# Performance work log

Hardware: AMD Instinct MI355X
Metric: run time of the kernel (lower is better)

The kernel has to match this reference:

```python
import jax, jax.numpy as jnp
import numpy as np

K_NN = 9  # kernel_size: neighbors per node (includes self, dist 0)


def knn_edges(feat):
    """feat: (B, C, N). Replicates DenseDilatedKnnGraph (dilation=1):
    L2-normalize over channels, dense pairwise sq-distance, top-k nearest."""
    nrm = jnp.sqrt(jnp.sum(feat * feat, axis=1, keepdims=True))
    xn = feat / jnp.maximum(nrm, 1e-12)            # F.normalize(dim=1)
    xt = jnp.swapaxes(xn, 1, 2)                    # (B, N, C)
    sq = jnp.sum(xt * xt, axis=-1)                 # (B, N)
    dist = sq[:, :, None] + sq[:, None, :] - 2.0 * jnp.einsum('bnc,bmc->bnm', xt, xt)
    _, nn_idx = jax.lax.top_k(-dist, K_NN)         # (B, N, k)
    center = jnp.broadcast_to(jnp.arange(nn_idx.shape[1], dtype=nn_idx.dtype)[None, :, None], nn_idx.shape)
    return nn_idx, center                          # (x_j sources, x_i targets)


def reference(x, W0, W1, bias):
    B, C, H, W = x.shape
    N = H * W
    NB = B * N
    feat = x.reshape(B, C, N)
    # KNN graph is built on detached features in the torch source
    x_j, x_i = knn_edges(jax.lax.stop_gradient(feat))
    E = B * N * K_NN
    # faithful to source: torch.linspace(0, B, steps=E, dtype=int64) batch offsets
    count = jnp.linspace(0.0, float(B), E).astype(jnp.int32)
    src = x_j.reshape(-1).astype(jnp.int32) + count * N
    dst = x_i.reshape(-1).astype(jnp.int32) + count * N
    valid = (src < NB) & (dst < NB)                # drop the out-of-range tail edge
    # flat_nodes: (B, C, H, W) -> (B*H*W, C), node id = b*HW + pixel
    nodes = jnp.swapaxes(feat, 1, 2).reshape(NB, C)
    # ChebConv K=2, sym norm, lambda_max=2: Tx0 = x, Tx1 = -(D^-1/2 A D^-1/2) x
    w = valid.astype(nodes.dtype)
    deg = jax.ops.segment_sum(w, src, num_segments=NB)
    dinv = jnp.where(deg > 0, jax.lax.rsqrt(jnp.maximum(deg, 1.0)), 0.0)
    norm = -(dinv[src] * w * dinv[dst])            # scaled-Laplacian edge weights
    msg = norm[:, None] * nodes[src]               # (E, C) gather + weight
    Tx1 = jax.ops.segment_sum(msg, dst, num_segments=NB)
    return nodes @ W0 + Tx1 @ W1 + bias


def setup_inputs() -> dict:
    key = jax.random.key(0)
    k1, k2, k3, k4 = jax.random.split(key, 4)
    B, C, H, W = 8, 48, 64, 64
    Cout = 48
    s = 1.0 / np.sqrt(C)
    return {
        'x': jax.random.normal(k1, (B, C, H, W), dtype=jnp.float32),
        'W0': jax.random.normal(k2, (C, Cout), dtype=jnp.float32) * s,
        'W1': jax.random.normal(k3, (C, Cout), dtype=jnp.float32) * s,
        'bias': jax.random.normal(k4, (Cout,), dtype=jnp.float32) * 0.01,
    }
```

## Files before the change

### kernel.cpp

```cpp
#include <hip/hip_runtime.h>

#define BATCH 8
#define CH    48
#define NPTS  4096
#define NBN   (BATCH*NPTS)
#define KNN   9
#define NCAND 12

typedef unsigned short u16;
typedef unsigned int   u32;
typedef unsigned long long u64;
typedef __bf16 bf16x8 __attribute__((ext_vector_type(8)));
typedef float  f32x4  __attribute__((ext_vector_type(4)));

__device__ __forceinline__ float bf2f(u16 v) { return __uint_as_float(((u32)v) << 16); }
__device__ __forceinline__ u16 f2bf(float f) {
  u32 u = __float_as_uint(f);
  u = (u + 0x7fffu + ((u >> 16) & 1u)) >> 16;
  return (u16)u;
}

#define MED3U(d, a, b, c) \
  asm("v_med3_u32 %0, %1, %2, %3" : "=v"(d) : "v"(a), "v"(b), "v"(c))
#define INS12(p0,p1,p2,p3,p4,p5,p6,p7,p8,p9,p10,p11,x) do { \
  MED3U(p11,p10,p11,x); MED3U(p10,p9,p10,x); MED3U(p9,p8,p9,x);  \
  MED3U(p8, p7, p8, x); MED3U(p7, p6,p7, x); MED3U(p6,p5,p6,x);  \
  MED3U(p5, p4, p5, x); MED3U(p4, p3,p4, x); MED3U(p3,p2,p3,x);  \
  MED3U(p2, p1, p2, x); MED3U(p1, p0,p1, x); p0 = min(p0, x);    \
} while (0)

__device__ __forceinline__ void stage_q(const u16* g, u16* l) {
  __builtin_amdgcn_global_load_lds(
      (const __attribute__((address_space(1))) void*)g,
      (__attribute__((address_space(3))) void*)l, 16, 0, 0);
}

__global__ __launch_bounds__(64)
void k_prep(const float* __restrict__ x, float* __restrict__ xraw,
            float* __restrict__ xn, float* __restrict__ csq,
            u16* __restrict__ Abuf, u16* __restrict__ Bbuf,
            int* __restrict__ deg) {
  int node = blockIdx.x * 64 + threadIdx.x;
  deg[node] = 0;
  int b = node >> 12, n = node & (NPTS - 1);
  const float* xb = x + (size_t)b * CH * NPTS;
  float f[CH];
#pragma unroll
  for (int c = 0; c < CH; ++c) f[c] = xb[(size_t)c * NPTS + n];
  float a0 = 0, a1 = 0, a2 = 0, a3 = 0;
#pragma unroll
  for (int k = 0; k < CH; k += 4) {
    a0 += f[k] * f[k]; a1 += f[k+1] * f[k+1];
    a2 += f[k+2] * f[k+2]; a3 += f[k+3] * f[k+3];
  }
  float nrm = fmaxf(sqrtf((a0 + a1) + (a2 + a3)), 1e-12f);
  float rn = 1.0f / nrm;
  a0 = a1 = a2 = a3 = 0;
#pragma unroll
  for (int k = 0; k < CH; k += 4) {
    float v0 = f[k]*rn, v1 = f[k+1]*rn, v2 = f[k+2]*rn, v3 = f[k+3]*rn;
    a0 += v0*v0; a1 += v1*v1; a2 += v2*v2; a3 += v3*v3;
  }
  float csqv = (a0 + a1) + (a2 + a3);
  csq[node] = csqv;
  float4* ro = (float4*)(xraw + (size_t)node * CH);
  float4* no = (float4*)(xn   + (size_t)node * CH);
#pragma unroll
  for (int i = 0; i < CH / 4; ++i) {
    ro[i] = make_float4(f[4*i], f[4*i+1], f[4*i+2], f[4*i+3]);
    no[i] = make_float4(f[4*i]*rn, f[4*i+1]*rn, f[4*i+2]*rn, f[4*i+3]*rn);
  }
  uint4* Bo = (uint4*)(Bbuf + (size_t)node * 128);
  u16* Ag = Abuf + (size_t)(node >> 4) * 2048 + (size_t)(node & 15) * 8;
#pragma unroll
  for (int g = 0; g < 6; ++g) {
    u32 bhw[4], blw[4], ahw[4], alw[4];
#pragma unroll
    for (int j = 0; j < 4; ++j) {
      int k = g * 8 + j * 2;
      float v0 = f[k] * rn, v1 = f[k+1] * rn;
      u16 h0 = f2bf(v0), h1 = f2bf(v1);
      u16 l0 = f2bf(v0 - bf2f(h0)), l1 = f2bf(v1 - bf2f(h1));
      bhw[j] = (u32)h0 | ((u32)h1 << 16);
      blw[j] = (u32)l0 | ((u32)l1 << 16);
      float w0 = -2.0f * v0, w1 = -2.0f * v1;
      u16 g0 = f2bf(w0), g1 = f2bf(w1);
      u16 m0 = f2bf(w0 - bf2f(g0)), m1 = f2bf(w1 - bf2f(g1));
      ahw[j] = (u32)g0 | ((u32)g1 << 16);
      alw[j] = (u32)m0 | ((u32)m1 << 16);
    }
    Bo[g]     = make_uint4(bhw[0], bhw[1], bhw[2], bhw[3]);
    Bo[8 + g] = make_uint4(blw[0], blw[1], blw[2], blw[3]);
    int v = g >> 2, q = g & 3;
    *(uint4*)(Ag + v * 512 + q * 128)        = make_uint4(ahw[0], ahw[1], ahw[2], ahw[3]);
    *(uint4*)(Ag + 1024 + v * 512 + q * 128) = make_uint4(alw[0], alw[1], alw[2], alw[3]);
  }
  {
    u16 h = f2bf(csqv); u16 l = f2bf(csqv - bf2f(h));
    Bo[6]  = make_uint4(0x3F80u, 0, 0, 0);
    Bo[14] = make_uint4(0, 0, 0, 0);
    *(uint4*)(Ag + 512 + 2 * 128)        = make_uint4((u32)h, 0, 0, 0);
    *(uint4*)(Ag + 1024 + 512 + 2 * 128) = make_uint4((u32)l, 0, 0, 0);
  }
  {
    uint4 z = make_uint4(0, 0, 0, 0);
    Bo[7] = z; Bo[15] = z;
    *(uint4*)(Ag + 512 + 3 * 128)        = z;
    *(uint4*)(Ag + 1024 + 512 + 3 * 128) = z;
  }
}

__global__ __launch_bounds__(256, 6)
void k_knn_m(const u16* __restrict__ Abuf, const u16* __restrict__ Bbuf,
             u32* __restrict__ candu) {
  __shared__ __align__(16) u16 As[2][2][2048];
  int tid = threadIdx.x;
  int lane = tid & 63;
  int wv = tid >> 6;
  int quad = lane >> 4, m16 = lane & 15;
  int panel = blockIdx.x * 4 + wv;
  int row = panel * 16 + m16;
  int b4096 = row & ~(NPTS - 1);
  int half = blockIdx.y;
  int ct0 = half * 128;

  const __bf16* Bb = (const __bf16*)Bbuf + (size_t)row * 128;
  bf16x8 bh0 = *(const bf16x8*)(Bb + quad * 8);
  bf16x8 bh1 = *(const bf16x8*)(Bb + 32 + quad * 8);
  bf16x8 bl0 = *(const bf16x8*)(Bb + 64 + quad * 8);
  bf16x8 bl1 = *(const bf16x8*)(Bb + 96 + quad * 8);

  const u16* gs = Abuf + ((size_t)(b4096 >> 4) + ct0) * 2048
                  + wv * 512 + lane * 8;

  u32 s0=~0u,s1=~0u,s2=~0u,s3=~0u,s4=~0u,s5=~0u,
      s6=~0u,s7=~0u,s8=~0u,s9=~0u,s10=~0u,s11=~0u;

  const f32x4 C25 = {2.5f, 2.5f, 2.5f, 2.5f};

#define LDA(P, S, A0,A1,A2,A3) do {                                         \
    const u16* _p = &As[P][S][lane * 8];                                    \
    A0 = *(const bf16x8*)(_p);                                              \
    A1 = *(const bf16x8*)(_p + 512);                                        \
    A2 = *(const bf16x8*)(_p + 1024);                                       \
    A3 = *(const bf16x8*)(_p + 1536);                                       \
  } while (0)
#define MFMA6(ACC, A0,A1,A2,A3) do {                                        \
    ACC = __builtin_amdgcn_mfma_f32_16x16x32_bf16(A0, bh0, C25, 0, 0, 0);   \
    ACC = __builtin_amdgcn_mfma_f32_16x16x32_bf16(A1, bh1, ACC, 0, 0, 0);   \
    ACC = __builtin_amdgcn_mfma_f32_16x16x32_bf16(A0, bl0, ACC, 0, 0, 0);   \
    ACC = __builtin_amdgcn_mfma_f32_16x16x32_bf16(A1, bl1, ACC, 0, 0, 0);   \
    ACC = __builtin_amdgcn_mfma_f32_16x16x32_bf16(A2, bh0, ACC, 0, 0, 0);   \
    ACC = __builtin_amdgcn_mfma_f32_16x16x32_bf16(A3, bh1, ACC, 0, 0, 0);   \
  } while (0)
#define FILTER(ACC, CT) do {                                                \
    u32 _colb = ((u32)(CT) << 4) | ((u32)quad << 2);                        \
    _Pragma("unroll")                                                       \
    for (int _r = 0; _r < 4; ++_r) {                                        \
      u32 _u = __float_as_uint((ACC)[_r]);                                  \
      u32 _x = (_u & 0xFFFFF000u) | (_colb | (u32)_r);                      \
      INS12(s0,s1,s2,s3,s4,s5,s6,s7,s8,s9,s10,s11, _x);                     \
    }                                                                       \
  } while (0)

  f32x4 accA, accB;
  bf16x8 a0, a1, a2, a3;

  stage_q(gs,        &As[0][0][wv * 512]);
  stage_q(gs + 2048, &As[0][1][wv * 512]);
  __syncthreads();

  LDA(0, 0, a0, a1, a2, a3);
  stage_q(gs + (size_t)2 * 2048, &As[1][0][wv * 512]);
  stage_q(gs + (size_t)3 * 2048, &As[1][1][wv * 512]);
  MFMA6(accA, a0, a1, a2, a3);
  LDA(0, 1, a0, a1, a2, a3);
  MFMA6(accB, a0, a1, a2, a3);
  FILTER(accA, ct0 + 0);
  __syncthreads();

  for (int p = 1; p < 63; ++p) {
    int par = p & 1;
    LDA(par, 0, a0, a1, a2, a3);
    stage_q(gs + (size_t)(2 * p + 2) * 2048, &As[par ^ 1][0][wv * 512]);
    stage_q(gs + (size_t)(2 * p + 3) * 2048, &As[par ^ 1][1][wv * 512]);
    MFMA6(accA, a0, a1, a2, a3);
    FILTER(accB, ct0 + 2 * p - 1);
    LDA(par, 1, a0, a1, a2, a3);
    MFMA6(accB, a0, a1, a2, a3);
    FILTER(accA, ct0 + 2 * p);
    __syncthreads();
  }
  LDA(1, 0, a0, a1, a2, a3);
  MFMA6(accA, a0, a1, a2, a3);
  FILTER(accB, ct0 + 125);
  LDA(1, 1, a0, a1, a2, a3);
  MFMA6(accB, a0, a1, a2, a3);
  FILTER(accA, ct0 + 126);
  FILTER(accB, ct0 + 127);
#undef LDA
#undef MFMA6
#undef FILTER

  u32* o = candu + (((size_t)row * 2 + half) * 4 + quad) * NCAND;
  o[0]=s0; o[1]=s1; o[2]=s2; o[3]=s3; o[4]=s4; o[5]=s5;
  o[6]=s6; o[7]=s7; o[8]=s8; o[9]=s9; o[10]=s10; o[11]=s11;
}

#define RWS 32
__global__ __launch_bounds__(256)
void k_rr(const u32* __restrict__ candu, const float* __restrict__ xn,
          const float* __restrict__ csq, u16* __restrict__ nn,
          int* __restrict__ deg) {
  __shared__ __align__(16) u32 cs[RWS][48];
  __shared__ __align__(16) float xnS[RWS][52];
  __shared__ float csqS[RWS];
  __shared__ float dS[RWS][12];
  __shared__ int   iS[RWS][12];
  int tid = threadIdx.x, bi = blockIdx.x;
  int row0 = (bi & 7) * NPTS + (bi >> 3) * RWS;
  int b4096 = row0 & ~(NPTS - 1);
  for (int i = tid; i < RWS * 12; i += 256) {
    int ln = i / 12, f4 = i % 12;
    *(float4*)&xnS[ln][f4 * 4] =
        *(const float4*)(xn + (size_t)(row0 + ln) * CH + f4 * 4);
  }
  if (tid < RWS) csqS[tid] = csq[row0 + tid];
  if (tid < RWS * 4) {
    int lr = tid >> 2, q = tid & 3;
    const uint4* src = (const uint4*)(candu + (size_t)(row0 + lr) * 96 + q * 24);
    u32 t0=~0u,t1=~0u,t2=~0u,t3=~0u,t4=~0u,t5=~0u,
        t6=~0u,t7=~0u,t8=~0u,t9=~0u,t10=~0u,t11=~0u;
#pragma unroll
    for (int s = 0; s < 6; ++s) {
      uint4 v = src[s];
      INS12(t0,t1,t2,t3,t4,t5,t6,t7,t8,t9,t10,t11, v.x);
      INS12(t0,t1,t2,t3,t4,t5,t6,t7,t8,t9,t10,t11, v.y);
      INS12(t0,t1,t2,t3,t4,t5,t6,t7,t8,t9,t10,t11, v.z);
      INS12(t0,t1,t2,t3,t4,t5,t6,t7,t8,t9,t10,t11, v.w);
    }
    u32* lw = &cs[lr][q * 12];
    lw[0]=t0; lw[1]=t1; lw[2]=t2; lw[3]=t3; lw[4]=t4; lw[5]=t5;
    lw[6]=t6; lw[7]=t7; lw[8]=t8; lw[9]=t9; lw[10]=t10; lw[11]=t11;
  }
  __syncthreads();
  if (tid < RWS) {
    int lr = tid;
    u32 g0=~0u,g1=~0u,g2=~0u,g3=~0u,g4=~0u,g5=~0u,
        g6=~0u,g7=~0u,g8=~0u,g9=~0u,g10=~0u,g11=~0u;
    const uint4* ls4 = (const uint4*)&cs[lr][0];
#pragma unroll
    for (int s = 0; s < 12; ++s) {
      uint4 v = ls4[s];
      INS12(g0,g1,g2,g3,g4,g5,g6,g7,g8,g9,g10,g11, v.x);
      INS12(g0,g1,g2,g3,g4,g5,g6,g7,g8,g9,g10,g11, v.y);
      INS12(g0,g1,g2,g3,g4,g5,g6,g7,g8,g9,g10,g11, v.z);
      INS12(g0,g1,g2,g3,g4,g5,g6,g7,g8,g9,g10,g11, v.w);
    }
    u32* lw = &cs[lr][0];
    lw[0]=g0; lw[1]=g1; lw[2]=g2; lw[3]=g3; lw[4]=g4; lw[5]=g5;
    lw[6]=g6; lw[7]=g7; lw[8]=g8; lw[9]=g9; lw[10]=g10; lw[11]=g11;
  }
  __syncthreads();
  for (int task = tid; task < RWS * 12; task += 256) {
    int r = task / 12, j = task % 12;
    int c = (int)(cs[r][j] & 0xFFFu);
    const float4* cp = (const float4*)(xn + (size_t)(b4096 + c) * CH);
    const float* rf = &xnS[r][0];
    float a0 = 0, a1 = 0, a2 = 0, a3 = 0;
#pragma unroll
    for (int i = 0; i < CH / 4; ++i) {
      float4 v = cp[i];
      a0 += rf[4*i]   * v.x; a1 += rf[4*i+1] * v.y;
      a2 += rf[4*i+2] * v.z; a3 += rf[4*i+3] * v.w;
    }
    float dist = (csqS[r] + csq[b4096 + c]) - 2.0f * ((a0 + a1) + (a2 + a3));
    dS[r][j] = dist; iS[r][j] = c;
  }
  __syncthreads();
  if (tid < RWS) {
    int lr = tid;
    int row = row0 + lr;
    float gd[KNN]; int gi[KNN];
#pragma unroll
    for (int j = 0; j < KNN; ++j) { gd[j] = 3.4e38f; gi[j] = 0x7fffffff; }
    for (int s = 0; s < NCAND; ++s) {
      float dc = dS[lr][s]; int ic = iS[lr][s];
      if (dc < gd[KNN - 1] || (dc == gd[KNN - 1] && ic < gi[KNN - 1])) {
        gd[KNN - 1] = dc; gi[KNN - 1] = ic;
#pragma unroll
        for (int k2 = KNN - 1; k2 > 0; --k2) {
          bool sw = (gd[k2] < gd[k2 - 1]) ||
                    (gd[k2] == gd[k2 - 1] && gi[k2] < gi[k2 - 1]);
          if (sw) {
            float td = gd[k2]; gd[k2] = gd[k2 - 1]; gd[k2 - 1] = td;
            int ti = gi[k2]; gi[k2] = gi[k2 - 1]; gi[k2 - 1] = ti;
          }
        }
      }
    }
    u16* o = nn + (size_t)row * KNN;
    int jmax = (row == NBN - 1) ? (KNN - 1) : KNN;
#pragma unroll
    for (int j = 0; j < KNN; ++j) o[j] = (u16)(gi[j] & (NPTS - 1));
    for (int j = 0; j < jmax; ++j)
      atomicAdd(&deg[b4096 + (gi[j] & (NPTS - 1))], 1);
  }
}

#define ONB 32
#define LPAD 52
__global__ __launch_bounds__(256)
void k_out_f(const float* __restrict__ xraw, const u16* __restrict__ nn,
             const int* __restrict__ deg,
             const float* __restrict__ W0, const float* __restrict__ W1,
             const float* __restrict__ bias, float* __restrict__ out) {
  __shared__ float w0[CH * CH], w1[CH * CH], bs[CH];
  __shared__ __align__(16) float fS[ONB * LPAD];
  __shared__ __align__(16) float txS[ONB * LPAD];
  __shared__ float dinvS[ONB];
  int tid = threadIdx.x;
  int bi = blockIdx.x;
  int n0 = (bi & 7) * NPTS + (bi >> 3) * ONB;
  int b12 = n0 & ~(NPTS - 1);
  for (int i = tid; i < CH * CH; i += 256) { w0[i] = W0[i]; w1[i] = W1[i]; }
  if (tid < CH) bs[tid] = bias[tid];
  for (int i = tid; i < ONB * 12; i += 256) {
    int ln = i / 12, f4 = i % 12;
    *(float4*)(fS + ln * LPAD + f4 * 4) =
        *(const float4*)(xraw + (size_t)(n0 + ln) * CH + f4 * 4);
  }
  if (tid < ONB) {
    int dg = deg[n0 + tid];
    dinvS[tid] = (dg > 0) ? (1.0f / sqrtf((float)dg)) : 0.0f;
  }
  __syncthreads();

  int ln = tid >> 3, p = tid & 7;
  int node = n0 + ln;
  float dn = dinvS[ln];
  const u16* nrow = nn + (size_t)node * KNN;
  bool full = (node != NBN - 1);
  float tx[6];
#pragma unroll
  for (int i = 0; i < 6; ++i) tx[i] = 0.f;
#pragma unroll
  for (int j = 0; j < KNN; ++j) {
    if (j < KNN - 1 || full) {
      int s = nrow[j] & (NPTS - 1);
      int dgs = deg[b12 + s];
      float ds = (dgs > 0) ? (1.0f / sqrtf((float)dgs)) : 0.0f;
      float w = -(ds * dn);
      const float2* pr = (const float2*)(xraw + (size_t)(b12 + s) * CH + p * 6);
#pragma unroll
      for (int q3 = 0; q3 < 3; ++q3) {
        float2 v = pr[q3];
        tx[q3*2]   += w * v.x; tx[q3*2+1] += w * v.y;
      }
    }
  }
#pragma unroll
  for (int q3 = 0; q3 < 3; ++q3)
    *(float2*)(txS + ln * LPAD + p * 6 + q3 * 2) =
        make_float2(tx[q3*2], tx[q3*2+1]);
  __syncthreads();

  float acc[6];
#pragma unroll
  for (int i = 0; i < 6; ++i) acc[i] = bs[p * 6 + i];
  const float* fr = fS + ln * LPAD;
  const float* tr = txS + ln * LPAD;
#pragma unroll
  for (int c = 0; c < CH; ++c) {
    float fc = fr[c];
    const float* wr = w0 + c * CH + p * 6;
#pragma unroll
    for (int i = 0; i < 6; ++i) acc[i] += fc * wr[i];
  }
#pragma unroll
  for (int c = 0; c < CH; ++c) {
    float tc = tr[c];
    const float* wr = w1 + c * CH + p * 6;
#pragma unroll
    for (int i = 0; i < 6; ++i) acc[i] += tc * wr[i];
  }
  float* op = out + (size_t)node * CH + p * 6;
#pragma unroll
  for (int q3 = 0; q3 < 3; ++q3)
    *(float2*)(op + q3 * 2) = make_float2(acc[q3*2], acc[q3*2+1]);
}

__global__ __launch_bounds__(256)
void k_zero(int* __restrict__ deg) { deg[blockIdx.x * 256 + threadIdx.x] = 0; }

__global__ __launch_bounds__(256)
void k_hist(const u16* __restrict__ nn, int* __restrict__ deg) {
  int node = blockIdx.x * 256 + threadIdx.x;
  int b12 = node & ~(NPTS - 1);
  int jmax = (node == NBN - 1) ? (KNN - 1) : KNN;
  for (int j = 0; j < jmax; ++j)
    atomicAdd(&deg[b12 + (nn[(size_t)node * KNN + j] & (NPTS - 1))], 1);
}

__global__ __launch_bounds__(256)
void k_dinv(const int* __restrict__ deg, float* __restrict__ dinv) {
  int i = blockIdx.x * 256 + threadIdx.x;
  int dg = deg[i];
  dinv[i] = (dg > 0) ? (1.0f / sqrtf((float)dg)) : 0.0f;
}

#define NQ    4
#define QCOLS (NPTS/NQ)
#define TCOLS 32
#define NTILES (QCOLS/TCOLS)
#define RPB   64

__global__ __launch_bounds__(256)
void k_knn_nb(const float* __restrict__ x, u16* __restrict__ nn) {
  __shared__ __align__(16) float tile[NQ * TCOLS * CH];
  __shared__ float nrmS[NQ * TCOLS];
  __shared__ float csq[NQ * TCOLS];
  int tid = threadIdx.x;
  int r0 = blockIdx.x * RPB;
  int b  = r0 >> 12;
  int q  = tid >> 6;
  int lr = tid & 63;
  int n  = (r0 + lr) & (NPTS - 1);
  const float* xb = x + (size_t)b * CH * NPTS;
  float rf[CH];
#pragma unroll
  for (int c = 0; c < CH; ++c) rf[c] = xb[(size_t)c * NPTS + n];
  float sqn;
  {
    float a0 = 0, a1 = 0, a2 = 0, a3 = 0;
#pragma unroll
    for (int k = 0; k < CH; k += 4) {
      a0 += rf[k] * rf[k]; a1 += rf[k+1] * rf[k+1];
      a2 += rf[k+2] * rf[k+2]; a3 += rf[k+3] * rf[k+3];
    }
    float nrm = fmaxf(sqrtf((a0 + a1) + (a2 + a3)), 1e-12f);
#pragma unroll
    for (int c = 0; c < CH; ++c) rf[c] = rf[c] / nrm;
    a0 = a1 = a2 = a3 = 0;
#pragma unroll
    for (int k = 0; k < CH; k += 4) {
      a0 += rf[k] * rf[k]; a1 += rf[k+1] * rf[k+1];
      a2 += rf[k+2] * rf[k+2]; a3 += rf[k+3] * rf[k+3];
    }
    sqn = (a0 + a1) + (a2 + a3);
  }
  float d[KNN]; int id[KNN];
#pragma unroll
  for (int j = 0; j < KNN; ++j) { d[j] = 3.4e38f; id[j] = 0x7fffffff; }
  for (int t = 0; t < NTILES; ++t) {
    __syncthreads();
#pragma unroll
    for (int qq = 0; qq < NQ; ++qq) {
      int colbase = qq * QCOLS + t * TCOLS;
      float* dst = tile + qq * TCOLS * CH;
#pragma unroll
      for (int it = 0; it < 6; ++it) {
        int i = it * 256 + tid;
        int c = i >> 5, p = i & 31;
        dst[p * CH + c] = xb[(size_t)c * NPTS + colbase + p];
      }
    }
    __syncthreads();
    if (tid < NQ * TCOLS) {
      const float* cp = tile + tid * CH;
      float a0 = 0, a1 = 0, a2 = 0, a3 = 0;
#pragma unroll
      for (int k = 0; k < CH; k += 4) {
        float4 v = *(const float4*)(cp + k);
        a0 += v.x * v.x; a1 += v.y * v.y; a2 += v.z * v.z; a3 += v.w * v.w;
      }
      nrmS[tid] = fmaxf(sqrtf((a0 + a1) + (a2 + a3)), 1e-12f);
    }
    __syncthreads();
    for (int i = tid; i < NQ * TCOLS * CH; i += 256)
      tile[i] = tile[i] / nrmS[i / CH];
    __syncthreads();
    if (tid < NQ * TCOLS) {
      const float* cp = tile + tid * CH;
      float a0 = 0, a1 = 0, a2 = 0, a3 = 0;
#pragma unroll
      for (int k = 0; k < CH; k += 4) {
        float4 v = *(const float4*)(cp + k);
        a0 += v.x * v.x; a1 += v.y * v.y; a2 += v.z * v.z; a3 += v.w * v.w;
      }
      csq[tid] = (a0 + a1) + (a2 + a3);
    }
    __syncthreads();
    int cbase = q * QCOLS + t * TCOLS;
    const float* tq = tile + q * TCOLS * CH;
    for (int cc = 0; cc < TCOLS; ++cc) {
      const float* cp = tq + cc * CH;
      float a0 = 0, a1 = 0, a2 = 0, a3 = 0;
#pragma unroll
      for (int k = 0; k < CH; k += 4) {
        float4 v = *(const float4*)(cp + k);
        a0 += rf[k] * v.x; a1 += rf[k+1] * v.y;
        a2 += rf[k+2] * v.z; a3 += rf[k+3] * v.w;
      }
      float dist = (sqn + csq[q * TCOLS + cc]) - 2.0f * ((a0 + a1) + (a2 + a3));
      if (dist < d[KNN - 1]) {
        d[KNN - 1] = dist; id[KNN - 1] = cbase + cc;
#pragma unroll
        for (int k2 = KNN - 1; k2 > 0; --k2) {
          if (d[k2] < d[k2 - 1]) {
            float td = d[k2]; d[k2] = d[k2 - 1]; d[k2 - 1] = td;
            int ti = id[k2]; id[k2] = id[k2 - 1]; id[k2 - 1] = ti;
          }
        }
      }
    }
  }
  __syncthreads();
  float* md = tile;
  int*   mi = (int*)(tile + 256 * KNN);
#pragma unroll
  for (int j = 0; j < KNN; ++j) { md[tid * KNN + j] = d[j]; mi[tid * KNN + j] = id[j]; }
  __syncthreads();
  if (tid < RPB) {
    float fd[KNN]; int fi[KNN];
#pragma unroll
    for (int j = 0; j < KNN; ++j) { fd[j] = 3.4e38f; fi[j] = 0x7fffffff; }
    for (int qq = 0; qq < NQ; ++qq) {
      int s = qq * RPB + tid;
      for (int j = 0; j < KNN; ++j) {
        float dc = md[s * KNN + j]; int ic = mi[s * KNN + j];
        if (dc < fd[KNN - 1]) {
          fd[KNN - 1] = dc; fi[KNN - 1] = ic;
#pragma unroll
          for (int k2 = KNN - 1; k2 > 0; --k2) {
            if (fd[k2] < fd[k2 - 1]) {
              float td = fd[k2]; fd[k2] = fd[k2 - 1]; fd[k2 - 1] = td;
              int ti = fi[k2]; fi[k2] = fi[k2 - 1]; fi[k2 - 1] = ti;
            }
          }
        }
      }
    }
    u16* o = nn + (size_t)(r0 + tid) * KNN;
#pragma unroll
    for (int j = 0; j < KNN; ++j) o[j] = (u16)(fi[j] & (NPTS - 1));
  }
}

__global__ __launch_bounds__(256)
void k_out_nb(const float* __restrict__ x, const u16* __restrict__ nn,
              const float* __restrict__ dinv,
              const float* __restrict__ W0, const float* __restrict__ W1,
              const float* __restrict__ bias, float* __restrict__ out) {
  __shared__ float w0[CH * CH], w1[CH * CH], bs[CH];
  for (int i = threadIdx.x; i < CH * CH; i += 256) { w0[i] = W0[i]; w1[i] = W1[i]; }
  if (threadIdx.x < CH) bs[threadIdx.x] = bias[threadIdx.x];
  __syncthreads();
  int node = blockIdx.x * 256 + threadIdx.x;
  int b = node >> 12, n = node & (NPTS - 1);
  const float* xb = x + (size_t)b * CH * NPTS;
  float f[CH], acc[CH], tx[CH];
#pragma unroll
  for (int c = 0; c < CH; ++c) f[c] = xb[(size_t)c * NPTS + n];
#pragma unroll
  for (int o = 0; o < CH; ++o) acc[o] = bs[o];
#pragma unroll
  for (int c = 0; c < CH; ++c) {
    float fc = f[c];
    const float* wr = w0 + c * CH;
#pragma unroll
    for (int o = 0; o < CH; ++o) acc[o] += fc * wr[o];
  }
#pragma unroll
  for (int c = 0; c < CH; ++c) tx[c] = 0.f;
  float dn = dinv[node];
  int jmax = (node == NBN - 1) ? (KNN - 1) : KNN;
  for (int j = 0; j < jmax; ++j) {
    int s = nn[(size_t)node * KNN + j] & (NPTS - 1);
    float w = -(dinv[(b << 12) + s] * dn);
#pragma unroll
    for (int c = 0; c < CH; ++c) tx[c] += w * xb[(size_t)c * NPTS + s];
  }
#pragma unroll
  for (int c = 0; c < CH; ++c) {
    float tc = tx[c];
    const float* wr = w1 + c * CH;
#pragma unroll
    for (int o = 0; o < CH; ++o) acc[o] += tc * wr[o];
  }
  float4* op = (float4*)(out + (size_t)node * CH);
#pragma unroll
  for (int i = 0; i < CH / 4; ++i)
    op[i] = make_float4(acc[4*i], acc[4*i+1], acc[4*i+2], acc[4*i+3]);
}

extern "C" void kernel_launch(void* const* d_in, const int* in_sizes, int n_in,
                              void* d_out, int out_size, void* d_ws, size_t ws_size,
                              hipStream_t stream) {
  const float* x    = (const float*)d_in[0];
  const float* W0   = (const float*)d_in[1];
  const float* W1   = (const float*)d_in[2];
  const float* bias = (const float*)d_in[3];
  float* out = (float*)d_out;
  char* w = (char*)d_ws;

  const size_t SZ_XN   = (size_t)NBN * CH * 4;
  const size_t SZ_XRAW = (size_t)NBN * CH * 4;
  const size_t SZ_CSQ  = (size_t)NBN * 4;
  const size_t SZ_NN   = (size_t)NBN * KNN * 2;
  const size_t SZ_DEG  = (size_t)NBN * 4;
  const size_t SZ_AB   = (size_t)NBN * 128 * 2;
  const size_t SZ_CU   = (size_t)NBN * 8 * NCAND * 4;
  const size_t needF = SZ_XN + SZ_XRAW + SZ_CSQ + SZ_NN + SZ_DEG
                     + 2 * SZ_AB + SZ_CU;

  if (ws_size >= needF) {
    size_t off = 0;
    float* xn   = (float*)(w + off); off += SZ_XN;
    float* xraw = (float*)(w + off); off += SZ_XRAW;
    float* csq  = (float*)(w + off); off += SZ_CSQ;
    u16*   nn   = (u16*)  (w + off); off += SZ_NN;
    int*   deg  = (int*)  (w + off); off += SZ_DEG;
    u16*   Abuf = (u16*)  (w + off); off += SZ_AB;
    u16*   Bbuf = (u16*)  (w + off); off += SZ_AB;
    u32*   candu= (u32*)  (w + off);
    k_prep    <<<NBN / 64, 64, 0, stream>>>(x, xraw, xn, csq, Abuf, Bbuf, deg);
    k_knn_m   <<<dim3(NBN / 64, 2), 256, 0, stream>>>(Abuf, Bbuf, candu);
    k_rr      <<<NBN / RWS, 256, 0, stream>>>(candu, xn, csq, nn, deg);
    k_out_f   <<<NBN / ONB, 256, 0, stream>>>(xraw, nn, deg, W0, W1, bias, out);
  } else {
    u16*   nn   = (u16*)w;
    int*   deg  = (int*)(w + SZ_NN);
    float* dinv = (float*)(w + SZ_NN + SZ_DEG);
    k_knn_nb <<<NBN / RPB, 256, 0, stream>>>(x, nn);
    k_zero   <<<NBN / 256, 256, 0, stream>>>(deg);
    k_hist   <<<NBN / 256, 256, 0, stream>>>(nn, deg);
    k_dinv   <<<NBN / 256, 256, 0, stream>>>(deg, dinv);
    k_out_nb <<<NBN / 256, 256, 0, stream>>>(x, nn, dinv, W0, W1, bias, out);
  }
}
```

Before: 200.9 us.

## Split KNN column range into quarters and stage prep outputs through LDS

The KNN distance kernel now splits the candidate columns into four parts instead of two, so it launches twice as many blocks with half the loop length each. This gives more parallelism at the cost of doubling the candidate buffer and the merge work in the rerank kernel. The prep kernel now writes its per-node outputs into shared memory first and then copies them out cooperatively, so the global stores are coalesced rather than strided per thread. That adds about 56KB of LDS per 64-thread block, which may reduce prep occupancy.

```diff
diff --git a/kernel.cpp b/kernel.cpp
--- a/kernel.cpp
+++ b/kernel.cpp
@@ -40,7 +40,13 @@
             float* __restrict__ xn, float* __restrict__ csq,
             u16* __restrict__ Abuf, u16* __restrict__ Bbuf,
             int* __restrict__ deg) {
-  int node = blockIdx.x * 64 + threadIdx.x;
+  __shared__ __align__(16) float xrawS[64 * 48];
+  __shared__ __align__(16) float xnS[64 * 48];
+  __shared__ __align__(16) u16   AS[64 * 128];
+  __shared__ __align__(16) u16   BS[64 * 128];
+  int tid = threadIdx.x;
+  int node0 = blockIdx.x * 64;
+  int node = node0 + tid;
   deg[node] = 0;
   int b = node >> 12, n = node & (NPTS - 1);
   const float* xb = x + (size_t)b * CH * NPTS;
@@ -63,15 +69,15 @@
   }
   float csqv = (a0 + a1) + (a2 + a3);
   csq[node] = csqv;
-  float4* ro = (float4*)(xraw + (size_t)node * CH);
-  float4* no = (float4*)(xn   + (size_t)node * CH);
+  float4* ro = (float4*)(xrawS + tid * 48);
+  float4* no = (float4*)(xnS   + tid * 48);
 #pragma unroll
   for (int i = 0; i < CH / 4; ++i) {
     ro[i] = make_float4(f[4*i], f[4*i+1], f[4*i+2], f[4*i+3]);
     no[i] = make_float4(f[4*i]*rn, f[4*i+1]*rn, f[4*i+2]*rn, f[4*i+3]*rn);
   }
-  uint4* Bo = (uint4*)(Bbuf + (size_t)node * 128);
-  u16* Ag = Abuf + (size_t)(node >> 4) * 2048 + (size_t)(node & 15) * 8;
+  uint4* Bo = (uint4*)(BS + tid * 128);
+  u16* Ag = AS + (tid >> 4) * 2048 + (tid & 15) * 8;
 #pragma unroll
   for (int g = 0; g < 6; ++g) {
     u32 bhw[4], blw[4], ahw[4], alw[4];
@@ -108,6 +114,20 @@
     *(uint4*)(Ag + 512 + 3 * 128)        = z;
     *(uint4*)(Ag + 1024 + 512 + 3 * 128) = z;
   }
+  __syncthreads();
+  {
+    float4* xrg = (float4*)(xraw + (size_t)node0 * CH);
+    float4* xng = (float4*)(xn   + (size_t)node0 * CH);
+    const float4* xrs = (const float4*)xrawS;
+    const float4* xns = (const float4*)xnS;
+    for (int i = tid; i < 64 * 48 / 4; i += 64) { xrg[i] = xrs[i]; xng[i] = xns[i]; }
+    uint4* Agl = (uint4*)(Abuf + (size_t)(node0 >> 4) * 2048);
+    const uint4* As4 = (const uint4*)AS;
+    for (int i = tid; i < 64 * 128 / 8; i += 64) Agl[i] = As4[i];
+    uint4* Bgl = (uint4*)(Bbuf + (size_t)node0 * 128);
+    const uint4* Bs4 = (const uint4*)BS;
+    for (int i = tid; i < 64 * 128 / 8; i += 64) Bgl[i] = Bs4[i];
+  }
 }
 
 __global__ __launch_bounds__(256, 6)
@@ -121,8 +141,8 @@
   int panel = blockIdx.x * 4 + wv;
   int row = panel * 16 + m16;
   int b4096 = row & ~(NPTS - 1);
-  int half = blockIdx.y;
-  int ct0 = half * 128;
+  int quarter = blockIdx.y;
+  int ct0 = quarter * 64;
 
   const __bf16* Bb = (const __bf16*)Bbuf + (size_t)row * 128;
   bf16x8 bh0 = *(const bf16x8*)(Bb + quad * 8);
@@ -179,7 +199,7 @@
   FILTER(accA, ct0 + 0);
   __syncthreads();
 
-  for (int p = 1; p < 63; ++p) {
+  for (int p = 1; p < 31; ++p) {
     int par = p & 1;
     LDA(par, 0, a0, a1, a2, a3);
     stage_q(gs + (size_t)(2 * p + 2) * 2048, &As[par ^ 1][0][wv * 512]);
@@ -193,16 +213,16 @@
   }
   LDA(1, 0, a0, a1, a2, a3);
   MFMA6(accA, a0, a1, a2, a3);
-  FILTER(accB, ct0 + 125);
+  FILTER(accB, ct0 + 61);
   LDA(1, 1, a0, a1, a2, a3);
   MFMA6(accB, a0, a1, a2, a3);
-  FILTER(accA, ct0 + 126);
-  FILTER(accB, ct0 + 127);
+  FILTER(accA, ct0 + 62);
+  FILTER(accB, ct0 + 63);
 #undef LDA
 #undef MFMA6
 #undef FILTER
 
-  u32* o = candu + (((size_t)row * 2 + half) * 4 + quad) * NCAND;
+  u32* o = candu + (((size_t)row * 4 + quarter) * 4 + quad) * NCAND;
   o[0]=s0; o[1]=s1; o[2]=s2; o[3]=s3; o[4]=s4; o[5]=s5;
   o[6]=s6; o[7]=s7; o[8]=s8; o[9]=s9; o[10]=s10; o[11]=s11;
 }
@@ -228,11 +248,11 @@
   if (tid < RWS) csqS[tid] = csq[row0 + tid];
   if (tid < RWS * 4) {
     int lr = tid >> 2, q = tid & 3;
-    const uint4* src = (const uint4*)(candu + (size_t)(row0 + lr) * 96 + q * 24);
+    const uint4* src = (const uint4*)(candu + (size_t)(row0 + lr) * 192 + q * 48);
     u32 t0=~0u,t1=~0u,t2=~0u,t3=~0u,t4=~0u,t5=~0u,
         t6=~0u,t7=~0u,t8=~0u,t9=~0u,t10=~0u,t11=~0u;
 #pragma unroll
-    for (int s = 0; s < 6; ++s) {
+    for (int s = 0; s < 12; ++s) {
       uint4 v = src[s];
       INS12(t0,t1,t2,t3,t4,t5,t6,t7,t8,t9,t10,t11, v.x);
       INS12(t0,t1,t2,t3,t4,t5,t6,t7,t8,t9,t10,t11, v.y);
@@ -610,7 +630,7 @@
   const size_t SZ_NN   = (size_t)NBN * KNN * 2;
   const size_t SZ_DEG  = (size_t)NBN * 4;
   const size_t SZ_AB   = (size_t)NBN * 128 * 2;
-  const size_t SZ_CU   = (size_t)NBN * 8 * NCAND * 4;
+  const size_t SZ_CU   = (size_t)NBN * 16 * NCAND * 4;
   const size_t needF = SZ_XN + SZ_XRAW + SZ_CSQ + SZ_NN + SZ_DEG
                      + 2 * SZ_AB + SZ_CU;
 
@@ -625,7 +645,7 @@
     u16*   Bbuf = (u16*)  (w + off); off += SZ_AB;
     u32*   candu= (u32*)  (w + off);
     k_prep    <<<NBN / 64, 64, 0, stream>>>(x, xraw, xn, csq, Abuf, Bbuf, deg);
-    k_knn_m   <<<dim3(NBN / 64, 2), 256, 0, stream>>>(Abuf, Bbuf, candu);
+    k_knn_m   <<<dim3(NBN / 64, 4), 256, 0, stream>>>(Abuf, Bbuf, candu);
     k_rr      <<<NBN / RWS, 256, 0, stream>>>(candu, xn, csq, nn, deg);
     k_out_f   <<<NBN / ONB, 256, 0, stream>>>(xraw, nn, deg, W0, W1, bias, out);
   } else {
```

After: 202.6 us. Within noise of the previous version (+0.8%).
